# Kernel tuning notes

Measured on AMD Instinct MI355X. Metric: run time of the kernel, lower is better.

Reference implementation:

```python
import jax, jax.numpy as jnp
import numpy as np

ALPHA = 1.0
BETA = 0.5

B, N, E = 4096, 4096, 16384


def setup_inputs() -> dict:
    key = jax.random.key(0)
    k1, k2, k3, k4, k5 = jax.random.split(key, 5)
    outputs = jax.random.normal(k1, (B, N), dtype=jnp.float32)
    targets = jax.random.uniform(k2, (B, N), dtype=jnp.float32)
    # per-node level weight (equivalent to node_levels dict -> level_weights lookup)
    level_w = jax.random.uniform(k3, (N,), dtype=jnp.float32)
    edge_src = jax.random.randint(k4, (E,), 0, N, dtype=jnp.int32)  # parent i
    edge_dst = jax.random.randint(k5, (E,), 0, N, dtype=jnp.int32)  # child  j
    return {"outputs": outputs, "targets": targets, "level_w": level_w,
            "edge_src": edge_src, "edge_dst": edge_dst}


def reference(outputs, targets, level_w, edge_src, edge_dst):
    # BCEWithLogits, reduction='none': softplus(x) - x*t (numerically stable)
    bce = jax.nn.softplus(outputs) - outputs * targets          # [B, N]
    weighted_bce = bce * level_w[None, :]                        # [B, N]

    probs = jax.nn.sigmoid(outputs)                              # [B, N]
    # for each edge (i=parent, j=child): consistency[:, j] += relu(p[:, j] - p[:, i])
    diff = jax.nn.relu(probs[:, edge_dst] - probs[:, edge_src])  # [B, E]
    consistency = jnp.zeros_like(probs).at[:, edge_dst].add(diff)  # [B, N]

    return ALPHA * weighted_bce.mean() + BETA * consistency.mean()
```

## Files before the change

kernel.cpp:

```cpp
#include <hip/hip_runtime.h>
#include <math.h>


#define ALPHA_C 1.0f
#define BETA_C  0.5f

constexpr int B = 4096;
constexpr int N = 4096;
constexpr int E = 16384;

typedef _Float16 h8 __attribute__((ext_vector_type(8)));

__global__ __launch_bounds__(64) void init_out_kernel(float* out) {
    if (threadIdx.x == 0) out[0] = 0.0f;
}

__device__ __forceinline__ void fast_sig_sp(float x, float& p, float& sp) {
    float q = __expf(-fabsf(x));
    float d = 1.0f + q;
    float r = __builtin_amdgcn_rcpf(d);
    p  = (x >= 0.0f) ? r : q * r;
    sp = fmaxf(x, 0.0f) + __logf(d);
}

constexpr int T1 = 1024;
__global__ __launch_bounds__(T1, 4)
__attribute__((amdgpu_waves_per_eu(4, 4)))
void k1_bce_sig(
    const float* __restrict__ outputs,
    const float* __restrict__ targets,
    const float* __restrict__ level_w,
    _Float16*    __restrict__ Pint,
    float*       __restrict__ out)
{
    __shared__ float red[16];
    const int g   = blockIdx.x;
    const int tid = threadIdx.x;

    const float4* out4 = (const float4*)outputs;
    const float4* tgt4 = (const float4*)targets;

    float4 xs[8], ts[8];
#pragma unroll
    for (int r = 0; r < 8; ++r) {
        const size_t off = (size_t)(8 * g + r) * (N / 4) + tid;
        xs[r] = out4[off];
        ts[r] = tgt4[off];
    }
    const float4 w = ((const float4*)level_w)[tid];
    const float wv[4] = {w.x, w.y, w.z, w.w};

    float s1 = 0.0f;
    h8 pv[4];
#pragma unroll
    for (int r = 0; r < 8; ++r) {
        const float xv[4] = {xs[r].x, xs[r].y, xs[r].z, xs[r].w};
        const float tv[4] = {ts[r].x, ts[r].y, ts[r].z, ts[r].w};
#pragma unroll
        for (int k = 0; k < 4; ++k) {
            float p, sp;
            fast_sig_sp(xv[k], p, sp);
            s1 = fmaf(wv[k], sp - xv[k] * tv[k], s1);
            pv[k][r] = (_Float16)p;
        }
    }
    h8* PG = (h8*)(Pint + (size_t)g * (N * 8));
#pragma unroll
    for (int k = 0; k < 4; ++k) PG[4 * tid + k] = pv[k];

#pragma unroll
    for (int off = 32; off > 0; off >>= 1) s1 += __shfl_down(s1, off, 64);
    const int wave = tid >> 6, lane = tid & 63;
    if (lane == 0) red[wave] = s1;
    __syncthreads();
    if (tid == 0) {
        float a = 0.0f;
#pragma unroll
        for (int i = 0; i < 16; ++i) a += red[i];
        atomicAdd(out, ALPHA_C * a / ((float)B * (float)N));
    }
}

constexpr int T2 = 1024;
__global__ __launch_bounds__(T2, 4) void k2_edges(
    const _Float16* __restrict__ Pint,
    const int*      __restrict__ edge_src,
    const int*      __restrict__ edge_dst,
    float*          __restrict__ out)
{
    __shared__ h8 Pl[N];
    __shared__ float red[16];

    const int g   = blockIdx.x;
    const int tid = threadIdx.x;

    const int4* es4 = (const int4*)edge_src;
    const int4* ed4 = (const int4*)edge_dst;
    int4 sc[4], dc[4];
#pragma unroll
    for (int j = 0; j < 4; ++j) {
        sc[j] = es4[tid + j * T2];
        dc[j] = ed4[tid + j * T2];
    }

    const h8* PG = (const h8*)(Pint + (size_t)g * (N * 8));
#pragma unroll
    for (int j = 0; j < N / T2; ++j)
        Pl[tid + j * T2] = PG[tid + j * T2];
    __syncthreads();

    float s2 = 0.0f;
    const h8 zero = {0, 0, 0, 0, 0, 0, 0, 0};
#pragma unroll
    for (int j = 0; j < 4; ++j) {
        h8 acc = zero;
        h8 a0 = Pl[sc[j].x], c0 = Pl[dc[j].x];
        h8 a1 = Pl[sc[j].y], c1 = Pl[dc[j].y];
        h8 a2 = Pl[sc[j].z], c2 = Pl[dc[j].z];
        h8 a3 = Pl[sc[j].w], c3 = Pl[dc[j].w];
        acc += __builtin_elementwise_max(c0 - a0, zero);
        acc += __builtin_elementwise_max(c1 - a1, zero);
        acc += __builtin_elementwise_max(c2 - a2, zero);
        acc += __builtin_elementwise_max(c3 - a3, zero);
#pragma unroll
        for (int l = 0; l < 8; ++l) s2 += (float)acc[l];
    }

#pragma unroll
    for (int off = 32; off > 0; off >>= 1) s2 += __shfl_down(s2, off, 64);
    const int wave = tid >> 6, lane = tid & 63;
    if (lane == 0) red[wave] = s2;
    __syncthreads();
    if (tid == 0) {
        float c = 0.0f;
#pragma unroll
        for (int i = 0; i < 16; ++i) c += red[i];
        atomicAdd(out, BETA_C * c / ((float)B * (float)N));
    }
}

extern "C" void kernel_launch(void* const* d_in, const int* in_sizes, int n_in,
                              void* d_out, int out_size, void* d_ws, size_t ws_size,
                              hipStream_t stream) {
    const float* outputs = (const float*)d_in[0];
    const float* targets = (const float*)d_in[1];
    const float* level_w = (const float*)d_in[2];
    const int*   edge_src = (const int*)d_in[3];
    const int*   edge_dst = (const int*)d_in[4];
    float* out = (float*)d_out;
    _Float16* Pint = (_Float16*)d_ws;

    init_out_kernel<<<1, 64, 0, stream>>>(out);
    k1_bce_sig<<<B / 8, T1, 0, stream>>>(outputs, targets, level_w, Pint, out);
    k2_edges<<<B / 8, T2, 0, stream>>>(Pint, edge_src, edge_dst, out);
}
```

Before: 177.8 us.

## Store probabilities row-major and transpose into interleaved layout inside edge kernel

The BCE/sigmoid kernel becomes a grid-stride kernel with 256-thread blocks and 2048 blocks. It writes fp16 probabilities in plain row-major layout, so it no longer has to gather 8 rows per thread. The edge kernel now reads 8 rows and transposes them in registers into the 8-row interleaved shared-memory layout. This moves the interleaving cost from the first kernel to the second. The aim is better occupancy and memory parallelism in the bandwidth-bound first kernel, at the price of extra register shuffling and a lower occupancy hint in the edge kernel.

```diff
diff --git a/kernel.cpp b/kernel.cpp
--- a/kernel.cpp
+++ b/kernel.cpp
@@ -9,6 +9,7 @@
 constexpr int N = 4096;
 constexpr int E = 16384;
 
+typedef _Float16 h4 __attribute__((ext_vector_type(4)));
 typedef _Float16 h8 __attribute__((ext_vector_type(8)));
 
 __global__ __launch_bounds__(64) void init_out_kernel(float* out) {
@@ -23,67 +24,60 @@
     sp = fmaxf(x, 0.0f) + __logf(d);
 }
 
-constexpr int T1 = 1024;
-__global__ __launch_bounds__(T1, 4)
-__attribute__((amdgpu_waves_per_eu(4, 4)))
-void k1_bce_sig(
+constexpr int T1  = 256;
+constexpr int G1  = 2048;
+constexpr int IT1 = (B * (N / 4)) / (T1 * G1);
+
+__global__ __launch_bounds__(T1, 8) void k1_bce_sig(
     const float* __restrict__ outputs,
     const float* __restrict__ targets,
     const float* __restrict__ level_w,
-    _Float16*    __restrict__ Pint,
+    _Float16*    __restrict__ P,
     float*       __restrict__ out)
 {
-    __shared__ float red[16];
-    const int g   = blockIdx.x;
-    const int tid = threadIdx.x;
-
+    __shared__ float red[4];
+    const int gt = blockIdx.x * T1 + threadIdx.x;
+    const int c  = gt & (N / 4 - 1);
+    const int r0 = gt >> 10;
     const float4* out4 = (const float4*)outputs;
     const float4* tgt4 = (const float4*)targets;
-
-    float4 xs[8], ts[8];
-#pragma unroll
-    for (int r = 0; r < 8; ++r) {
-        const size_t off = (size_t)(8 * g + r) * (N / 4) + tid;
-        xs[r] = out4[off];
-        ts[r] = tgt4[off];
-    }
-    const float4 w = ((const float4*)level_w)[tid];
+    const float4 w = ((const float4*)level_w)[c];
     const float wv[4] = {w.x, w.y, w.z, w.w};
+    h4* P4 = (h4*)P;
 
     float s1 = 0.0f;
-    h8 pv[4];
 #pragma unroll
-    for (int r = 0; r < 8; ++r) {
-        const float xv[4] = {xs[r].x, xs[r].y, xs[r].z, xs[r].w};
-        const float tv[4] = {ts[r].x, ts[r].y, ts[r].z, ts[r].w};
+    for (int s = 0; s < IT1; ++s) {
+        const size_t idx = (size_t)(r0 + s * (B / IT1)) * (N / 4) + c;
+        const float4 x = out4[idx];
+        const float4 t = tgt4[idx];
+        const float xv[4] = {x.x, x.y, x.z, x.w};
+        const float tv[4] = {t.x, t.y, t.z, t.w};
+        h4 pv;
 #pragma unroll
         for (int k = 0; k < 4; ++k) {
             float p, sp;
             fast_sig_sp(xv[k], p, sp);
             s1 = fmaf(wv[k], sp - xv[k] * tv[k], s1);
-            pv[k][r] = (_Float16)p;
+            pv[k] = (_Float16)p;
         }
+        P4[idx] = pv;
     }
-    h8* PG = (h8*)(Pint + (size_t)g * (N * 8));
-#pragma unroll
-    for (int k = 0; k < 4; ++k) PG[4 * tid + k] = pv[k];
 
 #pragma unroll
     for (int off = 32; off > 0; off >>= 1) s1 += __shfl_down(s1, off, 64);
-    const int wave = tid >> 6, lane = tid & 63;
+    const int wave = threadIdx.x >> 6, lane = threadIdx.x & 63;
     if (lane == 0) red[wave] = s1;
     __syncthreads();
-    if (tid == 0) {
-        float a = 0.0f;
-#pragma unroll
-        for (int i = 0; i < 16; ++i) a += red[i];
+    if (threadIdx.x == 0) {
+        float a = red[0] + red[1] + red[2] + red[3];
         atomicAdd(out, ALPHA_C * a / ((float)B * (float)N));
     }
 }
 
 constexpr int T2 = 1024;
-__global__ __launch_bounds__(T2, 4) void k2_edges(
-    const _Float16* __restrict__ Pint,
+__global__ __launch_bounds__(T2, 2) void k2_edges(
+    const _Float16* __restrict__ P,
     const int*      __restrict__ edge_src,
     const int*      __restrict__ edge_dst,
     float*          __restrict__ out)
@@ -103,10 +97,19 @@
         dc[j] = ed4[tid + j * T2];
     }
 
-    const h8* PG = (const h8*)(Pint + (size_t)g * (N * 8));
+    const h4* Pr = (const h4*)P + (size_t)(8 * g) * (N / 4);
+    h4 rowv[8];
 #pragma unroll
-    for (int j = 0; j < N / T2; ++j)
-        Pl[tid + j * T2] = PG[tid + j * T2];
+    for (int r = 0; r < 8; ++r)
+        rowv[r] = Pr[(size_t)r * (N / 4) + tid];
+    h8 tp[4];
+#pragma unroll
+    for (int k = 0; k < 4; ++k) {
+#pragma unroll
+        for (int r = 0; r < 8; ++r) tp[k][r] = rowv[r][k];
+    }
+#pragma unroll
+    for (int k = 0; k < 4; ++k) Pl[4 * tid + k] = tp[k];
     __syncthreads();
 
     float s2 = 0.0f;
@@ -148,9 +151,9 @@
     const int*   edge_src = (const int*)d_in[3];
     const int*   edge_dst = (const int*)d_in[4];
     float* out = (float*)d_out;
-    _Float16* Pint = (_Float16*)d_ws;
+    _Float16* P = (_Float16*)d_ws;
 
     init_out_kernel<<<1, 64, 0, stream>>>(out);
-    k1_bce_sig<<<B / 8, T1, 0, stream>>>(outputs, targets, level_w, Pint, out);
-    k2_edges<<<B / 8, T2, 0, stream>>>(Pint, edge_src, edge_dst, out);
+    k1_bce_sig<<<G1, T1, 0, stream>>>(outputs, targets, level_w, P, out);
+    k2_edges<<<B / 8, T2, 0, stream>>>(P, edge_src, edge_dst, out);
 }
```

Measured after the change: 179.8 us. Within noise of the previous version (+1.1%).
